# Kernel optimization log

Measured on AMD Instinct MI355X. Metric: run time of the kernel, lower is better.

The kernel has to match this reference:

```python
import jax, jax.numpy as jnp
import numpy as np
from jax import lax

B, C, H, W = 4, 256, 64, 64
EPS = 1e-5  # BatchNorm eps (eval mode)


def _bn(x, g, b, m, v):
    # eval-mode BatchNorm2d over channel dim
    inv = lax.rsqrt(v + EPS)
    return (x - m[None, :, None, None]) * (g * inv)[None, :, None, None] + b[None, :, None, None]


def _conv1x1(x, w, b):
    # w: [O, I]
    return jnp.einsum('oc,bchw->bohw', w, x) + b[None, :, None, None]


def _conv3x3(x, w, b):
    # w: [O, I, 3, 3], padding 'same'
    y = lax.conv_general_dilated(x, w, (1, 1), 'SAME',
                                 dimension_numbers=('NCHW', 'OIHW', 'NCHW'))
    return y + b[None, :, None, None]


def setup_inputs():
    key = jax.random.key(0)
    ks = jax.random.split(key, 12)
    s = 0.05
    Ch = C // 2
    d = {
        'inputs_0': jax.random.normal(ks[0], (B, C, H, W), jnp.float32),
        'inputs_1': jax.random.normal(ks[1], (B, C, H, W), jnp.float32),
        # 1x1 projections (conv0/conv1/conv2): C -> C/2
        'w_q': jax.random.normal(ks[2], (Ch, C), jnp.float32) * s,
        'b_q': jnp.zeros((Ch,), jnp.float32),
        'w_k': jax.random.normal(ks[3], (Ch, C), jnp.float32) * s,
        'b_k': jnp.zeros((Ch,), jnp.float32),
        'w_v': jax.random.normal(ks[4], (Ch, C), jnp.float32) * s,
        'b_v': jnp.zeros((Ch,), jnp.float32),
        # conv3: C/2 -> C (1x1)
        'w_o': jax.random.normal(ks[5], (C, Ch), jnp.float32) * s,
        'b_o': jnp.zeros((C,), jnp.float32),
        # batch_conv0
        'bn0_g': jnp.ones((C,), jnp.float32), 'bn0_b': jnp.zeros((C,), jnp.float32),
        'bn0_m': jnp.zeros((C,), jnp.float32), 'bn0_v': jnp.ones((C,), jnp.float32),
        # conv_block(2C -> C): conv0 3x3
        'cb_w0': jax.random.normal(ks[6], (C, 2 * C, 3, 3), jnp.float32) * s,
        'cb_b0': jnp.zeros((C,), jnp.float32),
        'cb_bn0_g': jnp.ones((C,), jnp.float32), 'cb_bn0_b': jnp.zeros((C,), jnp.float32),
        'cb_bn0_m': jnp.zeros((C,), jnp.float32), 'cb_bn0_v': jnp.ones((C,), jnp.float32),
        # conv_block conv1 3x3: C -> C
        'cb_w1': jax.random.normal(ks[7], (C, C, 3, 3), jnp.float32) * s,
        'cb_b1': jnp.zeros((C,), jnp.float32),
        'cb_bn1_g': jnp.ones((C,), jnp.float32), 'cb_bn1_b': jnp.zeros((C,), jnp.float32),
        'cb_bn1_m': jnp.zeros((C,), jnp.float32), 'cb_bn1_v': jnp.ones((C,), jnp.float32),
    }
    return d


def reference(inputs_0, inputs_1, w_q, b_q, w_k, b_k, w_v, b_v, w_o, b_o,
              bn0_g, bn0_b, bn0_m, bn0_v,
              cb_w0, cb_b0, cb_bn0_g, cb_bn0_b, cb_bn0_m, cb_bn0_v,
              cb_w1, cb_b1, cb_bn1_g, cb_bn1_b, cb_bn1_m, cb_bn1_v):
    b, c, h, w = inputs_0.shape
    ch = c // 2
    n = h * w
    # 1x1 projections
    x1 = _conv1x1(inputs_0, w_q, b_q).reshape(b, ch, n)   # conv0(inputs_0)
    x2 = _conv1x1(inputs_0, w_k, b_k).reshape(b, ch, n)   # conv1(inputs_0)
    x3 = _conv1x1(inputs_1, w_v, b_v).reshape(b, ch, n)   # conv2(inputs_1)
    # spatial cross-attention: [b, n, n] affinity, contraction over channels
    aff = jnp.einsum('bij,bik->bjk', x2, x3)              # [b, n, n]
    aff = jax.nn.softmax(aff, axis=-2)                    # softmax over dim j (rows)
    x0 = jnp.einsum('bij,bjk->bik', x1, aff)              # [b, ch, n]
    x0 = x0.reshape(b, ch, h, w)
    # output projection + BN + GELU (exact erf gelu, matching torch default)
    x0 = jax.nn.gelu(_bn(_conv1x1(x0, w_o, b_o), bn0_g, bn0_b, bn0_m, bn0_v), approximate=False)
    # conv_block on concat
    y = jnp.concatenate([x0, inputs_0], axis=1)           # [b, 2c, h, w]
    y = jax.nn.gelu(_bn(_conv3x3(y, cb_w0, cb_b0), cb_bn0_g, cb_bn0_b, cb_bn0_m, cb_bn0_v), approximate=False)
    y = jax.nn.gelu(_bn(_conv3x3(y, cb_w1, cb_b1), cb_bn1_g, cb_bn1_b, cb_bn1_m, cb_bn1_v), approximate=False)
    # AdaptiveMaxPool2d((1,1)) == global spatial max, then squeeze -> [b, c]
    out = jnp.max(y + x0, axis=(2, 3))
    return out
```

## Files before the change

### kernel.cpp

```cpp
#include <hip/hip_runtime.h>
#include <math.h>

#define B_ 4
#define C_ 256
#define CH_ 128
#define NN 4096

typedef __bf16 bf16x8 __attribute__((ext_vector_type(8)));
typedef float f32x16 __attribute__((ext_vector_type(16)));
typedef unsigned int u32;

__device__ __forceinline__ float gelu_erf(float x) {
    return 0.5f * x * (1.0f + erff(x * 0.7071067811865476f));
}

__device__ __forceinline__ u32 pkbf(float a, float b) {
    union { __bf16 h[2]; u32 u; } x;
    x.h[0] = (__bf16)a; x.h[1] = (__bf16)b;
    return x.u;
}

__global__ __launch_bounds__(256) void nhwc_cast2_kernel(
    const float* __restrict__ in0, const float* __restrict__ in1,
    __bf16* __restrict__ Xt0, __bf16* __restrict__ Xin1)
{
    __shared__ float Lt[64][65];
    const int t = threadIdx.x;
    const int p0 = blockIdx.x * 64;
    const int c0 = blockIdx.y * 64;
    const int z = blockIdx.z;
    const int b = z & 3;
    const float* src; __bf16* dst; int colbase, rowstride;
    if (z < 4) { src = in0; dst = Xt0; colbase = 256; rowstride = 512; }
    else       { src = in1; dst = Xin1; colbase = 0;  rowstride = 256; }
#pragma unroll
    for (int i = 0; i < 16; ++i) {
        int idx = t + i * 256;
        int c = idx >> 6, p = idx & 63;
        Lt[c][p] = src[((size_t)(b * 256 + c0 + c)) * 4096 + p0 + p];
    }
    __syncthreads();
#pragma unroll
    for (int i = 0; i < 16; ++i) {
        int idx = t + i * 256;
        int p = idx >> 6, c = idx & 63;
        dst[((size_t)(b * 4096 + p0 + p)) * rowstride + colbase + c0 + c] = (__bf16)Lt[c][p];
    }
}

__global__ __launch_bounds__(256) void wtrans_kernel(
    const float* __restrict__ w0, const float* __restrict__ w1,
    const float* __restrict__ wq, const float* __restrict__ wk,
    const float* __restrict__ wv, const float* __restrict__ wo,
    __bf16* __restrict__ Wt0, __bf16* __restrict__ Wt1,
    __bf16* __restrict__ wqb, __bf16* __restrict__ wkb,
    __bf16* __restrict__ wvb, __bf16* __restrict__ wob)
{
    int id = blockIdx.x * 256 + threadIdx.x;
    if (id < 131072) {
        int o = id >> 9, ci = id & 511;
        const float* s = w0 + (size_t)id * 9;
        const int chunk = ci >> 4, f = o >> 5;
        const int lane = (o & 31) + 32 * ((ci >> 3) & 1);
        const int j = ci & 7;
#pragma unroll
        for (int k = 0; k < 9; ++k)
            Wt0[((size_t)(chunk * 9 + k) * 8 + f) * 512 + lane * 8 + j] = (__bf16)s[k];
    } else if (id < 196608) {
        int id2 = id - 131072;
        int o = id2 >> 8, ci = id2 & 255;
        const float* s = w1 + (size_t)id2 * 9;
        const int chunk = ci >> 4, f = o >> 5;
        const int lane = (o & 31) + 32 * ((ci >> 3) & 1);
        const int j = ci & 7;
#pragma unroll
        for (int k = 0; k < 9; ++k)
            Wt1[((size_t)(chunk * 9 + k) * 8 + f) * 512 + lane * 8 + j] = (__bf16)s[k];
    } else {
        int id3 = id - 196608;
        int sel = id3 >> 15;
        int k = id3 & 32767;
        const float* s = sel == 0 ? wq : sel == 1 ? wk : sel == 2 ? wv : wo;
        __bf16* d = sel == 0 ? wqb : sel == 1 ? wkb : sel == 2 ? wvb : wob;
        d[k] = (__bf16)s[k];
    }
}

__global__ __launch_bounds__(256) void proj_mfma_kernel(
    const __bf16* __restrict__ Xt0,
    const __bf16* __restrict__ Xin1,
    const __bf16* __restrict__ wqb, const __bf16* __restrict__ wkb,
    const __bf16* __restrict__ wvb,
    const float* __restrict__ bq, const float* __restrict__ bk,
    const float* __restrict__ bv,
    __bf16* __restrict__ Vswz, __bf16* __restrict__ Kswz, __bf16* __restrict__ Qswz)
{
    __shared__ __align__(16) __bf16 Vt[4][64][80];
    __shared__ float biasl[128];

    const int t = threadIdx.x;
    const int which = blockIdx.z % 3;
    const int b = blockIdx.z / 3;
    const int p0 = blockIdx.x * 128;

    const __bf16* W = which == 0 ? wqb : which == 1 ? wkb : wvb;
    const float* bias = which == 0 ? bq : which == 1 ? bk : bv;
    const __bf16* src; int stride, colb;
    if (which == 2) { src = Xin1 + (size_t)b * NN * 256; stride = 256; colb = 0; }
    else            { src = Xt0  + (size_t)b * NN * 512; stride = 512; colb = 256; }

    if (t < 128) biasl[t] = bias[t];
    __syncthreads();

    const int lane = t & 63, w = t >> 6;
    const int l31 = lane & 31, hi = lane >> 5;
    const int wo2 = w >> 1, wp2 = w & 1;
    const int ob = wo2 * 64;
    const int pb = p0 + wp2 * 64;

    f32x16 acc[2][2];
#pragma unroll
    for (int i = 0; i < 2; ++i)
#pragma unroll
        for (int j = 0; j < 2; ++j)
#pragma unroll
            for (int e = 0; e < 16; ++e) acc[i][j][e] = 0.f;

#pragma unroll
    for (int kc = 0; kc < 16; ++kc) {
        bf16x8 a0 = *(const bf16x8*)&W[(size_t)(ob + l31) * 256 + hi * 8 + kc * 16];
        bf16x8 a1 = *(const bf16x8*)&W[(size_t)(ob + 32 + l31) * 256 + hi * 8 + kc * 16];
        bf16x8 b0 = *(const bf16x8*)&src[(size_t)(pb + l31) * stride + colb + hi * 8 + kc * 16];
        bf16x8 b1 = *(const bf16x8*)&src[(size_t)(pb + 32 + l31) * stride + colb + hi * 8 + kc * 16];
        acc[0][0] = __builtin_amdgcn_mfma_f32_32x32x16_bf16(a0, b0, acc[0][0], 0, 0, 0);
        acc[0][1] = __builtin_amdgcn_mfma_f32_32x32x16_bf16(a0, b1, acc[0][1], 0, 0, 0);
        acc[1][0] = __builtin_amdgcn_mfma_f32_32x32x16_bf16(a1, b0, acc[1][0], 0, 0, 0);
        acc[1][1] = __builtin_amdgcn_mfma_f32_32x32x16_bf16(a1, b1, acc[1][1], 0, 0, 0);
    }

    if (which) {
        __bf16* dst = (which == 1 ? Kswz : Qswz) + (size_t)b * NN * CH_;
#pragma unroll
        for (int mi = 0; mi < 2; ++mi)
#pragma unroll
            for (int nx = 0; nx < 2; ++nx) {
                const int tile = (pb >> 5) + nx;
#pragma unroll
                for (int q4 = 0; q4 < 4; ++q4) {
                    const int ic = (ob >> 4) + mi * 2 + (q4 >> 1);
                    const int og = ob + mi * 32 + q4 * 8 + hi * 4;
                    __bf16 pk[4];
#pragma unroll
                    for (int j = 0; j < 4; ++j)
                        pk[j] = (__bf16)(acc[mi][nx][q4 * 4 + j] + biasl[og + j]);
                    const size_t el = ((size_t)(tile * 8 + ic) * 64
                                       + l31 + 32 * (q4 & 1)) * 8 + hi * 4;
                    *(uint2*)&dst[el] = *(const uint2*)pk;
                }
            }
    } else {
#pragma unroll
        for (int mi = 0; mi < 2; ++mi)
#pragma unroll
            for (int nx = 0; nx < 2; ++nx) {
                const int ploc = nx * 32 + l31;
#pragma unroll
                for (int q4 = 0; q4 < 4; ++q4) {
                    const int oloc = mi * 32 + q4 * 8 + hi * 4;
#pragma unroll
                    for (int j = 0; j < 4; ++j)
                        Vt[w][oloc + j][ploc] =
                            (__bf16)(acc[mi][nx][q4 * 4 + j] + biasl[ob + oloc + j]);
                }
            }
        __syncthreads();
        __bf16* dst = Vswz + (size_t)b * NN * CH_;
#pragma unroll
        for (int s = 0; s < 8; ++s) {
            const int tl = s >> 2, jc = (s >> 1) & 1, il = s & 1;
            const int tile_g = (pb >> 5) + tl;
            const int icf_g = (ob >> 5) + il;
            const int i_loc = il * 32 + l31;
            const int kk = tl * 32 + jc * 16 + hi * 8;
            uint4 v = *(const uint4*)&Vt[w][i_loc][kk];
            const size_t el = ((size_t)((tile_g * 2 + jc) * 4 + icf_g) * 64 + lane) * 8;
            *(uint4*)&dst[el] = v;
        }
    }
}

__global__ __launch_bounds__(256, 4) void attn_mfma_kernel(
    const __bf16* __restrict__ Qswz, const __bf16* __restrict__ Kswz,
    const __bf16* __restrict__ Vswz,
    __bf16* __restrict__ Opart, float* __restrict__ Mpart, float* __restrict__ Lpart)
{
    __shared__ __bf16 Op[4][128][34];
    __shared__ float Ml[4][32], Ll[4][32];

    const int t = threadIdx.x;
    const int lane = t & 63;
    const int w = t >> 6;
    const int l31 = lane & 31;
    const int hi = lane >> 5;

    const int bid = blockIdx.x;
    const int xcd = bid & 7;
    const int b = xcd >> 1;
    const int local = bid >> 3;
    const int qt = (xcd & 1) * 64 + (local & 63);
    const int half = local >> 6;
    const int q0 = qt * 32;

    const __bf16* Qs = Qswz + (size_t)b * NN * CH_ + (size_t)qt * 4096 + lane * 8;
    bf16x8 qf[8];
#pragma unroll
    for (int ic = 0; ic < 8; ++ic) qf[ic] = *(const bf16x8*)(Qs + ic * 512);

    const __bf16* Ks = Kswz + (size_t)b * NN * CH_ + lane * 8;
    const __bf16* Vs = Vswz + (size_t)b * NN * CH_ + lane * 8;

    f32x16 oacc[4];
#pragma unroll
    for (int i = 0; i < 4; ++i)
#pragma unroll
        for (int e = 0; e < 16; ++e) oacc[i][e] = 0.f;

    float m = -3e38f, lsum = 0.f;
    const int tbase = half * 64 + w * 16;

    for (int jt = 0; jt < 16; ++jt) {
        const int tile = tbase + jt;
        f32x16 s;
#pragma unroll
        for (int e = 0; e < 16; ++e) s[e] = 0.f;
        const __bf16* Kt = Ks + (size_t)tile * 4096;
#pragma unroll
        for (int ic = 0; ic < 8; ++ic) {
            bf16x8 kf = *(const bf16x8*)(Kt + ic * 512);
            s = __builtin_amdgcn_mfma_f32_32x32x16_bf16(kf, qf[ic], s, 0, 0, 0);
        }
        float t8[8];
#pragma unroll
        for (int e = 0; e < 8; ++e) t8[e] = fmaxf(s[e], s[e + 8]);
#pragma unroll
        for (int e = 0; e < 4; ++e) t8[e] = fmaxf(t8[e], t8[e + 4]);
        t8[0] = fmaxf(t8[0], t8[2]); t8[1] = fmaxf(t8[1], t8[3]);
        float mu = fmaxf(t8[0], t8[1]);
        const float pm = fmaxf(mu, __shfl_xor(mu, 32));
        if (!__all(pm <= m + 8.f)) {
            const float mn = fmaxf(m, pm);
            const float al = __expf(m - mn);
            m = mn;
            lsum *= al;
#pragma unroll
            for (int i = 0; i < 4; ++i)
#pragma unroll
                for (int e = 0; e < 16; ++e) oacc[i][e] *= al;
        }
#pragma unroll
        for (int e = 0; e < 16; ++e) s[e] = __expf(s[e] - m);
        float s8[8];
#pragma unroll
        for (int e = 0; e < 8; ++e) s8[e] = s[e] + s[e + 8];
#pragma unroll
        for (int e = 0; e < 4; ++e) s8[e] += s8[e + 4];
        s8[0] += s8[2]; s8[1] += s8[3];
        float su = s8[0] + s8[1];
        lsum += su + __shfl_xor(su, 32);

        const __bf16* Vt = Vs + (size_t)tile * 4096;
        {
            u32 w0 = pkbf(s[0], s[1]), w1 = pkbf(s[2], s[3]);
            u32 w2 = pkbf(s[4], s[5]), w3 = pkbf(s[6], s[7]);
            asm("v_permlane32_swap_b32 %0, %1" : "+v"(w0), "+v"(w2));
            asm("v_permlane32_swap_b32 %0, %1" : "+v"(w1), "+v"(w3));
            union { u32 u4[4]; bf16x8 v; } pB;
            pB.u4[0] = w0; pB.u4[1] = w1; pB.u4[2] = w2; pB.u4[3] = w3;
#pragma unroll
            for (int icf = 0; icf < 4; ++icf) {
                bf16x8 vf = *(const bf16x8*)(Vt + icf * 512);
                oacc[icf] = __builtin_amdgcn_mfma_f32_32x32x16_bf16(vf, pB.v, oacc[icf], 0, 0, 0);
            }
        }
        {
            u32 w0 = pkbf(s[8], s[9]), w1 = pkbf(s[10], s[11]);
            u32 w2 = pkbf(s[12], s[13]), w3 = pkbf(s[14], s[15]);
            asm("v_permlane32_swap_b32 %0, %1" : "+v"(w0), "+v"(w2));
            asm("v_permlane32_swap_b32 %0, %1" : "+v"(w1), "+v"(w3));
            union { u32 u4[4]; bf16x8 v; } pB;
            pB.u4[0] = w0; pB.u4[1] = w1; pB.u4[2] = w2; pB.u4[3] = w3;
#pragma unroll
            for (int icf = 0; icf < 4; ++icf) {
                bf16x8 vf = *(const bf16x8*)(Vt + 2048 + icf * 512);
                oacc[icf] = __builtin_amdgcn_mfma_f32_32x32x16_bf16(vf, pB.v, oacc[icf], 0, 0, 0);
            }
        }
    }

#pragma unroll
    for (int icf = 0; icf < 4; ++icf)
#pragma unroll
        for (int q = 0; q < 16; ++q) {
            const int row = icf * 32 + (q & 3) + 8 * (q >> 2) + 4 * hi;
            Op[w][row][l31] = (__bf16)oacc[icf][q];
        }
    if (hi == 0) { Ml[w][l31] = m; Ll[w][l31] = lsum; }
    __syncthreads();
    {
        const int q = t & 31;
        const int i0g = (t >> 5) * 16;
        const float m0 = Ml[0][q], m1 = Ml[1][q], m2 = Ml[2][q], m3 = Ml[3][q];
        const float ms = fmaxf(fmaxf(m0, m1), fmaxf(m2, m3));
        const float a0 = __expf(m0 - ms), a1 = __expf(m1 - ms);
        const float a2 = __expf(m2 - ms), a3 = __expf(m3 - ms);
        const float den = a0 * Ll[0][q] + a1 * Ll[1][q] + a2 * Ll[2][q] + a3 * Ll[3][q];
        union { __bf16 h[16]; uint4 u4[2]; } pk;
#pragma unroll
        for (int ii = 0; ii < 16; ++ii) {
            const int i = i0g + ii;
            pk.h[ii] = (__bf16)(a0 * (float)Op[0][i][q] + a1 * (float)Op[1][i][q]
                              + a2 * (float)Op[2][i][q] + a3 * (float)Op[3][i][q]);
        }
        const size_t base = ((size_t)((half * 4 + b) * NN) + q0 + q) * CH_ + i0g;
        *(uint4*)&Opart[base] = pk.u4[0];
        *(uint4*)&Opart[base + 8] = pk.u4[1];
        if (t < 32) {
            Mpart[(size_t)(half * 4 + b) * NN + q0 + q] = ms;
            Lpart[(size_t)(half * 4 + b) * NN + q0 + q] = den;
        }
    }
}

__global__ __launch_bounds__(256) void attn_merge_kernel(
    const __bf16* __restrict__ Opart, const float* __restrict__ Mpart,
    const float* __restrict__ Lpart, __bf16* __restrict__ x0)
{
    const int id = blockIdx.x * 256 + threadIdx.x;
    const int qg = id >> 2;
    const int i0 = (id & 3) * 32;
    const int b = qg >> 12, q = qg & 4095;
    const size_t idx0 = (size_t)b * NN + q;
    const size_t idx1 = (size_t)(4 + b) * NN + q;
    const float m0 = Mpart[idx0], m1 = Mpart[idx1];
    const float ms = fmaxf(m0, m1);
    const float a0 = __expf(m0 - ms), a1 = __expf(m1 - ms);
    const float inv = 1.f / (a0 * Lpart[idx0] + a1 * Lpart[idx1]);
    const __bf16* O0 = &Opart[idx0 * CH_ + i0];
    const __bf16* O1 = &Opart[idx1 * CH_ + i0];
    union { __bf16 h[32]; uint4 u4[4]; } ov;
#pragma unroll
    for (int ii = 0; ii < 32; ++ii)
        ov.h[ii] = (__bf16)((a0 * (float)O0[ii] + a1 * (float)O1[ii]) * inv);
    uint4* dst = (uint4*)&x0[((size_t)b * NN + q) * CH_ + i0];
#pragma unroll
    for (int s = 0; s < 4; ++s) dst[s] = ov.u4[s];
}

__global__ __launch_bounds__(256) void convo_mfma_kernel(
    const __bf16* __restrict__ x0, const __bf16* __restrict__ wob,
    const float* __restrict__ bo,
    const float* __restrict__ g, const float* __restrict__ bb,
    const float* __restrict__ mm, const float* __restrict__ vv,
    __bf16* __restrict__ Xt0)
{
    __shared__ float scb[128], shb[128], bsb[128];
    const int t = threadIdx.x;
    const int p0 = blockIdx.x * 128;
    const int o0 = blockIdx.y * 128;
    const int b = blockIdx.z;
    if (t < 128) {
        const int o = o0 + t;
        const float sc = g[o] * rsqrtf(vv[o] + 1e-5f);
        scb[t] = sc; shb[t] = bb[o] - mm[o] * sc; bsb[t] = bo[o];
    }
    __syncthreads();

    const int lane = t & 63, w = t >> 6;
    const int l31 = lane & 31, hi = lane >> 5;
    const int wo2 = w >> 1, wp2 = w & 1;
    const int ob = o0 + wo2 * 64;
    const int pb = p0 + wp2 * 64;

    f32x16 acc[2][2];
#pragma unroll
    for (int i = 0; i < 2; ++i)
#pragma unroll
        for (int j = 0; j < 2; ++j)
#pragma unroll
            for (int e = 0; e < 16; ++e) acc[i][j][e] = 0.f;

#pragma unroll
    for (int kc = 0; kc < 8; ++kc) {
        bf16x8 a0 = *(const bf16x8*)&wob[(size_t)(ob + l31) * 128 + hi * 8 + kc * 16];
        bf16x8 a1 = *(const bf16x8*)&wob[(size_t)(ob + 32 + l31) * 128 + hi * 8 + kc * 16];
        bf16x8 b0 = *(const bf16x8*)&x0[((size_t)(b * NN) + pb + l31) * 128 + hi * 8 + kc * 16];
        bf16x8 b1 = *(const bf16x8*)&x0[((size_t)(b * NN) + pb + 32 + l31) * 128 + hi * 8 + kc * 16];
        acc[0][0] = __builtin_amdgcn_mfma_f32_32x32x16_bf16(a0, b0, acc[0][0], 0, 0, 0);
        acc[0][1] = __builtin_amdgcn_mfma_f32_32x32x16_bf16(a0, b1, acc[0][1], 0, 0, 0);
        acc[1][0] = __builtin_amdgcn_mfma_f32_32x32x16_bf16(a1, b0, acc[1][0], 0, 0, 0);
        acc[1][1] = __builtin_amdgcn_mfma_f32_32x32x16_bf16(a1, b1, acc[1][1], 0, 0, 0);
    }

#pragma unroll
    for (int mi = 0; mi < 2; ++mi)
#pragma unroll
        for (int nx = 0; nx < 2; ++nx) {
            const int p = pb + nx * 32 + l31;
            const size_t rowbase = ((size_t)(b * NN) + p) * 512 + o0;
#pragma unroll
            for (int q4 = 0; q4 < 4; ++q4) {
                const int ol = wo2 * 64 + mi * 32 + q4 * 8 + hi * 4;
                __bf16 pk[4];
#pragma unroll
                for (int j = 0; j < 4; ++j) {
                    float v = acc[mi][nx][q4 * 4 + j] + bsb[ol + j];
                    v = v * scb[ol + j] + shb[ol + j];
                    pk[j] = (__bf16)gelu_erf(v);
                }
                *(uint2*)&Xt0[rowbase + ol] = *(const uint2*)pk;
            }
        }
}

template<int IC, bool FUSEMAX>
__global__ __launch_bounds__(128) void conv3x3_mfma_kernel(
    const __bf16* __restrict__ Xsrc,
    const __bf16* __restrict__ Wf,
    const float* __restrict__ bias, const float* __restrict__ bng,
    const float* __restrict__ bnb, const float* __restrict__ bnm,
    const float* __restrict__ bnv,
    __bf16* __restrict__ out,
    const __bf16* __restrict__ Xg,
    float* __restrict__ part)
{
    constexpr int NC = IC / 16;
    __shared__ __align__(16) char Tl[2][6336];
    __shared__ float scb[64], shb[64], bsb[64];
    __shared__ float red[2][64];

    const int t = threadIdx.x;
    const int bid = blockIdx.x;
    const int xcd = bid & 7, local = bid >> 3;
    const int b = xcd >> 1, yhi = xcd & 1;
    const int y0 = yhi * 32 + (local & 31);
    const int m = local >> 5;
    const int o0 = m * 64;

    if (t < 64) {
        const int o = o0 + t;
        const float sc = bng[o] * rsqrtf(bnv[o] + 1e-5f);
        scb[t] = sc; shb[t] = bnb[o] - bnm[o] * sc; bsb[t] = bias[o];
    }

    const int lane = t & 63, w = t >> 6;
    const int l31 = lane & 31, hi = lane >> 5;

    uint4 ireg[3];

    auto loadI = [&](int c0) {
#pragma unroll
        for (int s = 0; s < 3; ++s) {
            int u = t + s * 128;
            int g = u & 1, x = (u >> 1) & 63, r = u >> 7;
            int yy = y0 - 1 + r;
            if (yy >= 0 && yy < 64)
                ireg[s] = *(const uint4*)&Xsrc[((size_t)(b * 4096 + yy * 64 + x)) * IC + c0 + g * 8];
            else
                ireg[s] = make_uint4(0u, 0u, 0u, 0u);
        }
    };
    auto writeI = [&](char* dst) {
#pragma unroll
        for (int s = 0; s < 3; ++s) {
            int u = t + s * 128;
            int g = u & 1, x = (u >> 1) & 63, r = u >> 7;
            int xh = x + 1;
            int byte = r * 2112 + ((xh * 32 + g * 16) ^ ((xh & 7) << 4));
            *(uint4*)(dst + byte) = ireg[s];
        }
        if (t < 12) {
            int g = t & 1, side = (t >> 1) & 1, r = t >> 2;
            int xh = side ? 65 : 0;
            int byte = r * 2112 + ((xh * 32 + g * 16) ^ ((xh & 7) << 4));
            *(uint4*)(dst + byte) = make_uint4(0u, 0u, 0u, 0u);
        }
    };

    const __bf16* Wb = Wf + ((size_t)(m * 2) * 64 + lane) * 8;
    bf16x8 wA[9][2];
    auto loadA = [&](int c) {
#pragma unroll
        for (int k9 = 0; k9 < 9; ++k9) {
            const __bf16* wp = Wb + (size_t)(c * 9 + k9) * 4096;
            wA[k9][0] = *(const bf16x8*)(wp);
            wA[k9][1] = *(const bf16x8*)(wp + 512);
        }
    };

    f32x16 acc[2];
#pragma unroll
    for (int i = 0; i < 2; ++i)
#pragma unroll
        for (int e = 0; e < 16; ++e) acc[i][e] = 0.f;

    int Boff[3];
#pragma unroll
    for (int dx = 0; dx < 3; ++dx) {
        int xh = w * 32 + l31 + dx;
        Boff[dx] = (xh * 32 + hi * 16) ^ ((xh & 7) << 4);
    }

    auto compute = [&](const char* Tb) {
#pragma unroll
        for (int k9 = 0; k9 < 9; ++k9) {
            const int dy = k9 / 3, dx = k9 % 3;
            bf16x8 bv = *(const bf16x8*)(Tb + dy * 2112 + Boff[dx]);
            acc[0] = __builtin_amdgcn_mfma_f32_32x32x16_bf16(wA[k9][0], bv, acc[0], 0, 0, 0);
            acc[1] = __builtin_amdgcn_mfma_f32_32x32x16_bf16(wA[k9][1], bv, acc[1], 0, 0, 0);
        }
    };

    loadI(0); loadA(0);
    writeI(Tl[0]);
    asm volatile("s_waitcnt lgkmcnt(0)" ::: "memory");
    __builtin_amdgcn_s_barrier();
    for (int c = 0; c < NC; ++c) {
        const int cur = c & 1;
        if (c + 1 < NC) loadI((c + 1) * 16);
        compute(Tl[cur]);
        if (c + 1 < NC) { loadA(c + 1); writeI(Tl[cur ^ 1]); }
        asm volatile("s_waitcnt lgkmcnt(0)" ::: "memory");
        __builtin_amdgcn_s_barrier();
    }

    const int p = y0 * 64 + w * 32 + l31;
    if constexpr (!FUSEMAX) {
        const size_t rowbase = ((size_t)(b * 4096 + p)) * 256 + o0;
#pragma unroll
        for (int mi = 0; mi < 2; ++mi)
#pragma unroll
            for (int q = 0; q < 4; ++q) {
                const int obase = mi * 32 + q * 8 + hi * 4;
                __bf16 pk[4];
#pragma unroll
                for (int j = 0; j < 4; ++j) {
                    float v = acc[mi][q * 4 + j] + bsb[obase + j];
                    v = v * scb[obase + j] + shb[obase + j];
                    pk[j] = (__bf16)gelu_erf(v);
                }
                *(uint2*)&out[rowbase + obase] = *(const uint2*)pk;
            }
    } else {
        const size_t xbase = ((size_t)(b * 4096 + p)) * 512 + o0;
#pragma unroll
        for (int mi = 0; mi < 2; ++mi)
#pragma unroll
            for (int q = 0; q < 4; ++q) {
                const int obase = mi * 32 + q * 8 + hi * 4;
                union { uint2 u; __bf16 h[4]; } xg;
                xg.u = *(const uint2*)&Xg[xbase + obase];
#pragma unroll
                for (int j = 0; j < 4; ++j) {
                    float v = acc[mi][q * 4 + j] + bsb[obase + j];
                    v = v * scb[obase + j] + shb[obase + j];
                    acc[mi][q * 4 + j] = gelu_erf(v) + (float)xg.h[j];
                }
            }
#pragma unroll
        for (int off = 1; off < 32; off <<= 1)
#pragma unroll
            for (int mi = 0; mi < 2; ++mi)
#pragma unroll
                for (int e = 0; e < 16; ++e)
                    acc[mi][e] = fmaxf(acc[mi][e], __shfl_xor(acc[mi][e], off));
        if (l31 == 0) {
#pragma unroll
            for (int mi = 0; mi < 2; ++mi)
#pragma unroll
                for (int q = 0; q < 4; ++q)
#pragma unroll
                    for (int j = 0; j < 4; ++j)
                        red[w][mi * 32 + q * 8 + hi * 4 + j] = acc[mi][q * 4 + j];
        }
        __syncthreads();
        if (t < 64)
            part[((size_t)(b * 64 + y0)) * 256 + o0 + t] = fmaxf(red[0][t], red[1][t]);
    }
}

__global__ __launch_bounds__(256) void maxfin_kernel(
    const float* __restrict__ part, float* __restrict__ out)
{
    const int o = threadIdx.x;
    const int b = blockIdx.x;
    float mx = -1e30f;
    for (int c = 0; c < 64; ++c)
        mx = fmaxf(mx, part[((size_t)(b * 64 + c)) * 256 + o]);
    out[b * 256 + o] = mx;
}

extern "C" void kernel_launch(void* const* d_in, const int* in_sizes, int n_in,
                              void* d_out, int out_size, void* d_ws, size_t ws_size,
                              hipStream_t stream)
{
    const float* in0  = (const float*)d_in[0];
    const float* in1  = (const float*)d_in[1];
    const float* w_q  = (const float*)d_in[2];
    const float* b_q  = (const float*)d_in[3];
    const float* w_k  = (const float*)d_in[4];
    const float* b_k  = (const float*)d_in[5];
    const float* w_v  = (const float*)d_in[6];
    const float* b_v  = (const float*)d_in[7];
    const float* w_o  = (const float*)d_in[8];
    const float* b_o  = (const float*)d_in[9];
    const float* bn0g = (const float*)d_in[10];
    const float* bn0b = (const float*)d_in[11];
    const float* bn0m = (const float*)d_in[12];
    const float* bn0v = (const float*)d_in[13];
    const float* cbw0 = (const float*)d_in[14];
    const float* cbb0 = (const float*)d_in[15];
    const float* cb0g = (const float*)d_in[16];
    const float* cb0b = (const float*)d_in[17];
    const float* cb0m = (const float*)d_in[18];
    const float* cb0v = (const float*)d_in[19];
    const float* cbw1 = (const float*)d_in[20];
    const float* cbb1 = (const float*)d_in[21];
    const float* cb1g = (const float*)d_in[22];
    const float* cb1b = (const float*)d_in[23];
    const float* cb1m = (const float*)d_in[24];
    const float* cb1v = (const float*)d_in[25];

    char* wsb = (char*)d_ws;
    const size_t MB = 1u << 20;
    __bf16* Xt0  = (__bf16*)(wsb);
    __bf16* Xin1 = (__bf16*)(wsb + 16 * MB);
    __bf16* Opart= (__bf16*)(wsb + 16 * MB);
    __bf16* Qswz = (__bf16*)(wsb + 24 * MB);
    __bf16* x0   = (__bf16*)(wsb + 24 * MB);
    __bf16* Kswz = (__bf16*)(wsb + 28 * MB);
    __bf16* y0   = (__bf16*)(wsb + 24 * MB);
    __bf16* Vswz = (__bf16*)(wsb + 32 * MB);
    __bf16* wqb  = (__bf16*)(wsb + 40 * MB);
    __bf16* wkb  = (__bf16*)(wsb + 40 * MB + 65536);
    __bf16* wvb  = (__bf16*)(wsb + 40 * MB + 2 * 65536);
    __bf16* wob  = (__bf16*)(wsb + 40 * MB + 3 * 65536);
    __bf16* Wt0  = (__bf16*)(wsb + 40 * MB + 4 * 65536);
    __bf16* Wt1  = (__bf16*)(wsb + 40 * MB + 4 * 65536 + 2359296);
    float*  Mpart= (float*)(wsb + 44 * MB);
    float*  Lpart= (float*)(wsb + 44 * MB + 131072);
    float*  part = (float*)(wsb + 44 * MB + 2 * 131072);
    float* outp = (float*)d_out;

    nhwc_cast2_kernel<<<dim3(64, 4, 8), 256, 0, stream>>>(in0, in1, Xt0, Xin1);
    wtrans_kernel<<<1280, 256, 0, stream>>>(cbw0, cbw1, w_q, w_k, w_v, w_o,
                                            Wt0, Wt1, wqb, wkb, wvb, wob);
    proj_mfma_kernel<<<dim3(32, 1, 12), 256, 0, stream>>>(
        Xt0, Xin1, wqb, wkb, wvb, b_q, b_k, b_v, Vswz, Kswz, Qswz);
    attn_mfma_kernel<<<1024, 256, 0, stream>>>(Qswz, Kswz, Vswz, Opart, Mpart, Lpart);
    attn_merge_kernel<<<256, 256, 0, stream>>>(Opart, Mpart, Lpart, x0);
    convo_mfma_kernel<<<dim3(32, 2, 4), 256, 0, stream>>>(
        x0, wob, b_o, bn0g, bn0b, bn0m, bn0v, Xt0);
    conv3x3_mfma_kernel<512, false><<<1024, 128, 0, stream>>>(
        Xt0, Wt0, cbb0, cb0g, cb0b, cb0m, cb0v, y0, nullptr, nullptr);
    conv3x3_mfma_kernel<256, true><<<1024, 128, 0, stream>>>(
        y0, Wt1, cbb1, cb1g, cb1b, cb1m, cb1v, nullptr, Xt0, part);
    maxfin_kernel<<<4, 256, 0, stream>>>(part, outp);
}
```

Before: 239.4 us.

## Store intermediate activations in channel-chunked NC16HW layout across kernels

Activation buffers change from pixel-major NHWC with a wide row stride to a blocked layout of 16-channel chunks, each holding all 4096 pixels contiguously. The cast, projection, output-conv and both 3x3 conv kernels are all updated to read and write this layout. Each 16-channel load in the conv inner loop now touches a contiguous span instead of rows strided by 512 or 256 elements. Epilogue stores, however, become scattered 8-byte writes across chunk planes, which may coalesce less well.

```diff
diff --git a/kernel.cpp b/kernel.cpp
--- a/kernel.cpp
+++ b/kernel.cpp
@@ -22,7 +22,7 @@
 
 __global__ __launch_bounds__(256) void nhwc_cast2_kernel(
     const float* __restrict__ in0, const float* __restrict__ in1,
-    __bf16* __restrict__ Xt0, __bf16* __restrict__ Xin1)
+    __bf16* __restrict__ Xt0c, __bf16* __restrict__ Xin1c)
 {
     __shared__ float Lt[64][65];
     const int t = threadIdx.x;
@@ -30,9 +30,9 @@
     const int c0 = blockIdx.y * 64;
     const int z = blockIdx.z;
     const int b = z & 3;
-    const float* src; __bf16* dst; int colbase, rowstride;
-    if (z < 4) { src = in0; dst = Xt0; colbase = 256; rowstride = 512; }
-    else       { src = in1; dst = Xin1; colbase = 0;  rowstride = 256; }
+    const float* src; __bf16* dst; int chbase, nch;
+    if (z < 4) { src = in0; dst = Xt0c;  chbase = 256; nch = 32; }
+    else       { src = in1; dst = Xin1c; chbase = 0;   nch = 16; }
 #pragma unroll
     for (int i = 0; i < 16; ++i) {
         int idx = t + i * 256;
@@ -44,7 +44,9 @@
     for (int i = 0; i < 16; ++i) {
         int idx = t + i * 256;
         int p = idx >> 6, c = idx & 63;
-        dst[((size_t)(b * 4096 + p0 + p)) * rowstride + colbase + c0 + c] = (__bf16)Lt[c][p];
+        const int ch = chbase + c0 + c;
+        dst[(((size_t)(b * nch + (ch >> 4)) * 4096) + p0 + p) * 16 + (ch & 15)]
+            = (__bf16)Lt[c][p];
     }
 }
 
@@ -87,8 +89,8 @@
 }
 
 __global__ __launch_bounds__(256) void proj_mfma_kernel(
-    const __bf16* __restrict__ Xt0,
-    const __bf16* __restrict__ Xin1,
+    const __bf16* __restrict__ Xt0c,
+    const __bf16* __restrict__ Xin1c,
     const __bf16* __restrict__ wqb, const __bf16* __restrict__ wkb,
     const __bf16* __restrict__ wvb,
     const float* __restrict__ bq, const float* __restrict__ bk,
@@ -105,9 +107,9 @@
 
     const __bf16* W = which == 0 ? wqb : which == 1 ? wkb : wvb;
     const float* bias = which == 0 ? bq : which == 1 ? bk : bv;
-    const __bf16* src; int stride, colb;
-    if (which == 2) { src = Xin1 + (size_t)b * NN * 256; stride = 256; colb = 0; }
-    else            { src = Xt0  + (size_t)b * NN * 512; stride = 512; colb = 256; }
+    const __bf16* src = (which == 2)
+        ? Xin1c + (size_t)b * 16 * 4096 * 16
+        : Xt0c  + ((size_t)(b * 32 + 16)) * 4096 * 16;
 
     if (t < 128) biasl[t] = bias[t];
     __syncthreads();
@@ -130,8 +132,8 @@
     for (int kc = 0; kc < 16; ++kc) {
         bf16x8 a0 = *(const bf16x8*)&W[(size_t)(ob + l31) * 256 + hi * 8 + kc * 16];
         bf16x8 a1 = *(const bf16x8*)&W[(size_t)(ob + 32 + l31) * 256 + hi * 8 + kc * 16];
-        bf16x8 b0 = *(const bf16x8*)&src[(size_t)(pb + l31) * stride + colb + hi * 8 + kc * 16];
-        bf16x8 b1 = *(const bf16x8*)&src[(size_t)(pb + 32 + l31) * stride + colb + hi * 8 + kc * 16];
+        bf16x8 b0 = *(const bf16x8*)&src[((size_t)kc * 4096 + pb + l31) * 16 + hi * 8];
+        bf16x8 b1 = *(const bf16x8*)&src[((size_t)kc * 4096 + pb + 32 + l31) * 16 + hi * 8];
         acc[0][0] = __builtin_amdgcn_mfma_f32_32x32x16_bf16(a0, b0, acc[0][0], 0, 0, 0);
         acc[0][1] = __builtin_amdgcn_mfma_f32_32x32x16_bf16(a0, b1, acc[0][1], 0, 0, 0);
         acc[1][0] = __builtin_amdgcn_mfma_f32_32x32x16_bf16(a1, b0, acc[1][0], 0, 0, 0);
@@ -361,7 +363,7 @@
     const float* __restrict__ bo,
     const float* __restrict__ g, const float* __restrict__ bb,
     const float* __restrict__ mm, const float* __restrict__ vv,
-    __bf16* __restrict__ Xt0)
+    __bf16* __restrict__ Xt0c)
 {
     __shared__ float scb[128], shb[128], bsb[128];
     const int t = threadIdx.x;
@@ -406,10 +408,10 @@
 #pragma unroll
         for (int nx = 0; nx < 2; ++nx) {
             const int p = pb + nx * 32 + l31;
-            const size_t rowbase = ((size_t)(b * NN) + p) * 512 + o0;
 #pragma unroll
             for (int q4 = 0; q4 < 4; ++q4) {
                 const int ol = wo2 * 64 + mi * 32 + q4 * 8 + hi * 4;
+                const int chg = o0 + ol;
                 __bf16 pk[4];
 #pragma unroll
                 for (int j = 0; j < 4; ++j) {
@@ -417,7 +419,8 @@
                     v = v * scb[ol + j] + shb[ol + j];
                     pk[j] = (__bf16)gelu_erf(v);
                 }
-                *(uint2*)&Xt0[rowbase + ol] = *(const uint2*)pk;
+                *(uint2*)&Xt0c[(((size_t)(b * 32 + (chg >> 4)) * 4096) + p) * 16 + (chg & 15)]
+                    = *(const uint2*)pk;
             }
         }
 }
@@ -457,14 +460,15 @@
 
     uint4 ireg[3];
 
-    auto loadI = [&](int c0) {
+    auto loadI = [&](int cc) {
+        const __bf16* base = Xsrc + ((size_t)(b * NC + cc)) * 4096 * 16;
 #pragma unroll
         for (int s = 0; s < 3; ++s) {
             int u = t + s * 128;
             int g = u & 1, x = (u >> 1) & 63, r = u >> 7;
             int yy = y0 - 1 + r;
             if (yy >= 0 && yy < 64)
-                ireg[s] = *(const uint4*)&Xsrc[((size_t)(b * 4096 + yy * 64 + x)) * IC + c0 + g * 8];
+                ireg[s] = *(const uint4*)&base[((size_t)(yy * 64 + x)) * 16 + g * 8];
             else
                 ireg[s] = make_uint4(0u, 0u, 0u, 0u);
         }
@@ -526,7 +530,7 @@
     __builtin_amdgcn_s_barrier();
     for (int c = 0; c < NC; ++c) {
         const int cur = c & 1;
-        if (c + 1 < NC) loadI((c + 1) * 16);
+        if (c + 1 < NC) loadI(c + 1);
         compute(Tl[cur]);
         if (c + 1 < NC) { loadA(c + 1); writeI(Tl[cur ^ 1]); }
         asm volatile("s_waitcnt lgkmcnt(0)" ::: "memory");
@@ -535,12 +539,12 @@
 
     const int p = y0 * 64 + w * 32 + l31;
     if constexpr (!FUSEMAX) {
-        const size_t rowbase = ((size_t)(b * 4096 + p)) * 256 + o0;
 #pragma unroll
         for (int mi = 0; mi < 2; ++mi)
 #pragma unroll
             for (int q = 0; q < 4; ++q) {
                 const int obase = mi * 32 + q * 8 + hi * 4;
+                const int chg = o0 + obase;
                 __bf16 pk[4];
 #pragma unroll
                 for (int j = 0; j < 4; ++j) {
@@ -548,17 +552,19 @@
                     v = v * scb[obase + j] + shb[obase + j];
                     pk[j] = (__bf16)gelu_erf(v);
                 }
-                *(uint2*)&out[rowbase + obase] = *(const uint2*)pk;
+                *(uint2*)&out[(((size_t)(b * 16 + (chg >> 4)) * 4096) + p) * 16 + (chg & 15)]
+                    = *(const uint2*)pk;
             }
     } else {
-        const size_t xbase = ((size_t)(b * 4096 + p)) * 512 + o0;
 #pragma unroll
         for (int mi = 0; mi < 2; ++mi)
 #pragma unroll
             for (int q = 0; q < 4; ++q) {
                 const int obase = mi * 32 + q * 8 + hi * 4;
+                const int chg = o0 + obase;
                 union { uint2 u; __bf16 h[4]; } xg;
-                xg.u = *(const uint2*)&Xg[xbase + obase];
+                xg.u = *(const uint2*)&Xg[(((size_t)(b * 32 + (chg >> 4)) * 4096) + p) * 16
+                                          + (chg & 15)];
 #pragma unroll
                 for (int j = 0; j < 4; ++j) {
                     float v = acc[mi][q * 4 + j] + bsb[obase + j];
@@ -632,8 +638,8 @@
 
     char* wsb = (char*)d_ws;
     const size_t MB = 1u << 20;
-    __bf16* Xt0  = (__bf16*)(wsb);
-    __bf16* Xin1 = (__bf16*)(wsb + 16 * MB);
+    __bf16* Xt0c = (__bf16*)(wsb);
+    __bf16* Xin1c= (__bf16*)(wsb + 16 * MB);
     __bf16* Opart= (__bf16*)(wsb + 16 * MB);
     __bf16* Qswz = (__bf16*)(wsb + 24 * MB);
     __bf16* x0   = (__bf16*)(wsb + 24 * MB);
@@ -651,18 +657,18 @@
     float*  part = (float*)(wsb + 44 * MB + 2 * 131072);
     float* outp = (float*)d_out;
 
-    nhwc_cast2_kernel<<<dim3(64, 4, 8), 256, 0, stream>>>(in0, in1, Xt0, Xin1);
+    nhwc_cast2_kernel<<<dim3(64, 4, 8), 256, 0, stream>>>(in0, in1, Xt0c, Xin1c);
     wtrans_kernel<<<1280, 256, 0, stream>>>(cbw0, cbw1, w_q, w_k, w_v, w_o,
                                             Wt0, Wt1, wqb, wkb, wvb, wob);
     proj_mfma_kernel<<<dim3(32, 1, 12), 256, 0, stream>>>(
-        Xt0, Xin1, wqb, wkb, wvb, b_q, b_k, b_v, Vswz, Kswz, Qswz);
+        Xt0c, Xin1c, wqb, wkb, wvb, b_q, b_k, b_v, Vswz, Kswz, Qswz);
     attn_mfma_kernel<<<1024, 256, 0, stream>>>(Qswz, Kswz, Vswz, Opart, Mpart, Lpart);
     attn_merge_kernel<<<256, 256, 0, stream>>>(Opart, Mpart, Lpart, x0);
     convo_mfma_kernel<<<dim3(32, 2, 4), 256, 0, stream>>>(
-        x0, wob, b_o, bn0g, bn0b, bn0m, bn0v, Xt0);
+        x0, wob, b_o, bn0g, bn0b, bn0m, bn0v, Xt0c);
     conv3x3_mfma_kernel<512, false><<<1024, 128, 0, stream>>>(
-        Xt0, Wt0, cbb0, cb0g, cb0b, cb0m, cb0v, y0, nullptr, nullptr);
+        Xt0c, Wt0, cbb0, cb0g, cb0b, cb0m, cb0v, y0, nullptr, nullptr);
     conv3x3_mfma_kernel<256, true><<<1024, 128, 0, stream>>>(
-        y0, Wt1, cbb1, cb1g, cb1b, cb1m, cb1v, nullptr, Xt0, part);
+        y0, Wt1, cbb1, cb1g, cb1b, cb1m, cb1v, nullptr, Xt0c, part);
     maxfin_kernel<<<4, 256, 0, stream>>>(part, outp);
 }
```

New measurement: 222.7 us (median of 2 runs). 7.0% less time.
